# Performance work log

Measured on AMD Instinct MI355X. Metric: run time of the kernel, lower is better.

## Reference

```python
import jax, jax.numpy as jnp
import numpy as np

N_NODES = 8192
N_FEATURES = 512
EMB = 128
N_HEADS = 4
EPS = 1e-6


def setup_inputs() -> dict:
    key = jax.random.key(0)
    k1, k2, k3 = jax.random.split(key, 3)
    X = jax.random.normal(k1, (N_NODES, N_FEATURES), dtype=jnp.float32)
    W = jax.random.normal(k2, (N_FEATURES, EMB), dtype=jnp.float32)
    Z = jax.random.normal(k3, (N_HEADS, N_NODES, EMB), dtype=jnp.float32)
    beta = jnp.ones((), dtype=jnp.float32)
    return {"X": X, "W": W, "Z": Z, "beta": beta}


def reference(X, W, Z, beta):
    # DenseLayer: node embedding
    X_emb = X @ W                                   # [N, E]
    # AffinityLayer: Z @ X_emb^T then cosine-style normalization
    aff = jnp.einsum('hne,me->hnm', Z, X_emb)       # [H, N, N]
    X_norm = jnp.linalg.norm(X_emb, axis=-1)        # [N]
    Z_norm = jnp.linalg.norm(Z, axis=-1)            # [H, N]
    aff = aff / (X_norm[None, None, :] + EPS)
    aff = aff / (Z_norm[:, :, None] + EPS)
    # PoolingLayer: max over heads
    aff = jnp.max(aff, axis=0)                      # [N, N]
    # undirected -> symmetrize
    aff = (aff + aff.T) / 2.0
    # ScalingLayer: map [-1,1] -> [0,1]
    aff = (aff + 1.0) / 2.0
    # ExponentiationLayer
    aff = jnp.power(aff, beta)
    return aff
```

## Files before the change

kernel.cpp:

```cpp
#include <hip/hip_runtime.h>
#include <stdint.h>
#include <stddef.h>

#define N_NODES 8192
#define N_FEAT  512
#define EMB     128
#define N_HEADS 4
#define TILE    128
#define TG      (N_NODES / TILE)
#define NPAIR   (TG * (TG + 1) / 2)
#define TILE_ELEMS (TILE * EMB)

typedef __attribute__((ext_vector_type(8)))  short bf16x8;
typedef __attribute__((ext_vector_type(16))) float f32x16;

__device__ __forceinline__ unsigned short f2bf(float f) {
  union { float f; unsigned int u; } x; x.f = f;
  unsigned int r = (x.u + 0x7FFFu + ((x.u >> 16) & 1u)) >> 16;
  return (unsigned short)r;
}
__device__ __forceinline__ float bf2f(unsigned short u) {
  union { unsigned int u; float f; } x; x.u = ((unsigned int)u) << 16;
  return x.f;
}

__device__ __forceinline__ void gl_lds16(const unsigned short* g, unsigned short* l) {
  __builtin_amdgcn_global_load_lds(
      (__attribute__((address_space(1))) void*)(void*)g,
      (__attribute__((address_space(3))) void*)l, 16, 0, 0);
}

__device__ __forceinline__ int swz_off(int r, int c) {
  int kc = c >> 3;
  return r * EMB + (((kc ^ (r & 7)) << 3) | (c & 7));
}

__device__ __forceinline__ int tidx(int r, int c) {
  int m = (r & 31) ^ ((r & 4) << 2);
  return r * 128 + (c ^ m);
}

__global__ void __launch_bounds__(512) xw_kernel(const float* __restrict__ X,
                                                 const float* __restrict__ W,
                                                 unsigned short* __restrict__ Xen) {
  __shared__ float xs[32][N_FEAT];
  const int t = threadIdx.x;
  const int row0 = blockIdx.x * 32;
#pragma unroll
  for (int i = 0; i < 8; ++i) {
    int e4 = i * 512 + t;
    int row = e4 >> 7;
    int col = (e4 & 127) * 4;
    *(float4*)&xs[row][col] = *(const float4*)&X[(size_t)(row0 + row) * N_FEAT + col];
  }
  __syncthreads();
  const int c0 = (t & 31) * 4;
  const int r0 = (t >> 5) * 2;
  float a00=0.f,a01=0.f,a02=0.f,a03=0.f,a10=0.f,a11=0.f,a12=0.f,a13=0.f;
  for (int k = 0; k < N_FEAT; k += 2) {
    float4 w0 = *(const float4*)&W[(size_t)k * EMB + c0];
    float4 w1 = *(const float4*)&W[(size_t)(k + 1) * EMB + c0];
    float x00 = xs[r0][k],     x01 = xs[r0][k + 1];
    float x10 = xs[r0 + 1][k], x11 = xs[r0 + 1][k + 1];
    a00 += x00*w0.x; a01 += x00*w0.y; a02 += x00*w0.z; a03 += x00*w0.w;
    a10 += x10*w0.x; a11 += x10*w0.y; a12 += x10*w0.z; a13 += x10*w0.w;
    a00 += x01*w1.x; a01 += x01*w1.y; a02 += x01*w1.z; a03 += x01*w1.w;
    a10 += x11*w1.x; a11 += x11*w1.y; a12 += x11*w1.z; a13 += x11*w1.w;
  }
  float s0 = a00*a00 + a01*a01 + a02*a02 + a03*a03;
  float s1 = a10*a10 + a11*a11 + a12*a12 + a13*a13;
#pragma unroll
  for (int off = 16; off >= 1; off >>= 1) {
    s0 += __shfl_xor(s0, off);
    s1 += __shfl_xor(s1, off);
  }
  float inv0 = 1.0f / (sqrtf(s0) + 1e-6f);
  float inv1 = 1.0f / (sqrtf(s1) + 1e-6f);
  union { unsigned short u[4]; uint2 v; } o0, o1;
  o0.u[0]=f2bf(a00*inv0); o0.u[1]=f2bf(a01*inv0); o0.u[2]=f2bf(a02*inv0); o0.u[3]=f2bf(a03*inv0);
  o1.u[0]=f2bf(a10*inv1); o1.u[1]=f2bf(a11*inv1); o1.u[2]=f2bf(a12*inv1); o1.u[3]=f2bf(a13*inv1);
  int n0 = row0 + r0;
  int t0 = n0 >> 7, rr0 = n0 & 127;
  int t1 = (n0 + 1) >> 7, rr1 = (n0 + 1) & 127;
  *(uint2*)&Xen[(size_t)t0 * TILE_ELEMS + swz_off(rr0, c0)] = o0.v;
  *(uint2*)&Xen[(size_t)t1 * TILE_ELEMS + swz_off(rr1, c0)] = o1.v;
}

__global__ void __launch_bounds__(256) znorm_kernel(const float* __restrict__ in,
                                                    unsigned short* __restrict__ out) {
  const int row = blockIdx.x * 4 + (threadIdx.x >> 6);
  const int lane = threadIdx.x & 63;
  float2 v = *(const float2*)&in[(size_t)row * EMB + lane * 2];
  float ss = v.x * v.x + v.y * v.y;
#pragma unroll
  for (int off = 32; off >= 1; off >>= 1) ss += __shfl_xor(ss, off);
  const float s = 1.0f / (sqrtf(ss) + 1e-6f);
  union { unsigned short u[2]; unsigned int w; } o;
  o.u[0] = f2bf(v.x * s);
  o.u[1] = f2bf(v.y * s);
  int tile = row >> 7, r = row & 127, c = lane * 2;
  *(unsigned int*)&out[(size_t)tile * TILE_ELEMS + swz_off(r, c)] = o.w;
}

__device__ __forceinline__ void stageZ(unsigned short* dstLds, const unsigned short* src,
                                       int wid, int lane) {
#pragma unroll
  for (int i = 0; i < 4; ++i) {
    int cbase = i * 512 + wid * 64;
    gl_lds16(src + (size_t)(cbase + lane) * 8, dstLds + (size_t)cbase * 8);
  }
}

__device__ __forceinline__ void do_stage(const unsigned short* cur, const bf16x8 (&XB)[8],
                                         f32x16 (&M)[2], int R0, int fr, int fh) {
  f32x16 acc0 = {}, acc1 = {};
  const int rb = R0 + fr;
  const int sw = rb & 7;
  const unsigned short* base0 = cur + rb * EMB;
#pragma unroll
  for (int kk = 0; kk < 8; ++kk) {
    int kc = kk * 2 + fh;
    int off = ((kc ^ sw) << 3);
    bf16x8 a0 = *(const bf16x8*)(base0 + off);
    bf16x8 a1 = *(const bf16x8*)(base0 + 32 * EMB + off);
    acc0 = __builtin_amdgcn_mfma_f32_32x32x16_bf16(a0, XB[kk], acc0, 0, 0, 0);
    acc1 = __builtin_amdgcn_mfma_f32_32x32x16_bf16(a1, XB[kk], acc1, 0, 0, 0);
  }
#pragma unroll
  for (int q = 0; q < 16; ++q) {
    M[0][q] = fmaxf(M[0][q], acc0[q]);
    M[1][q] = fmaxf(M[1][q], acc1[q]);
  }
}

__global__ void __launch_bounds__(512, 1) affinity_kernel(const unsigned short* __restrict__ Xen,
                                                          const unsigned short* __restrict__ Zn,
                                                          const float* __restrict__ betap,
                                                          float* __restrict__ out) {
  __shared__ __align__(16) unsigned short Zb[2][TILE_ELEMS];
  unsigned short* Tb = &Zb[0][0];

  int bid = blockIdx.x;
  int p = (bid & 7) * (NPAIR / 8) + (bid >> 3);
  int i = (int)(((float)(2 * TG + 1) -
                 sqrtf((float)((2 * TG + 1) * (2 * TG + 1) - 8 * p))) * 0.5f);
  if (i < 0) i = 0;
  if (i > TG - 1) i = TG - 1;
  while (i > 0 && i * TG - i * (i - 1) / 2 > p) --i;
  while ((i + 1) * TG - (i + 1) * i / 2 <= p) ++i;
  const int bi = i;
  const int bj = i + (p - (i * TG - i * (i - 1) / 2));
  const bool diag = (bi == bj);
  const int NS = diag ? 4 : 8;

  const int t = threadIdx.x;
  const int lane = t & 63;
  const int wid = t >> 6;
  const int R0 = (wid >> 2) * 64;
  const int C0 = (wid & 3) * 32;
  const int fr = lane & 31;
  const int fh = lane >> 5;

  stageZ(Zb[0], Zn + ((size_t)(0 * TG + bi) << 14), wid, lane);

  bf16x8 XjB[8], XiB[8];
  {
    const unsigned short* xj = Xen + ((size_t)bj << 14);
    const int r = C0 + fr;
    const int sw = r & 7;
#pragma unroll
    for (int kk = 0; kk < 8; ++kk) {
      int kc = kk * 2 + fh;
      XjB[kk] = *(const bf16x8*)&xj[r * EMB + ((kc ^ sw) << 3)];
    }
    if (!diag) {
      const unsigned short* xi = Xen + ((size_t)bi << 14);
#pragma unroll
      for (int kk = 0; kk < 8; ++kk) {
        int kc = kk * 2 + fh;
        XiB[kk] = *(const bf16x8*)&xi[r * EMB + ((kc ^ sw) << 3)];
      }
    }
  }

  f32x16 maxI[2], maxJ[2];
#pragma unroll
  for (int q = 0; q < 16; ++q) {
    maxI[0][q] = -3.0e38f; maxI[1][q] = -3.0e38f;
    maxJ[0][q] = -3.0e38f; maxJ[1][q] = -3.0e38f;
  }

  __syncthreads();

#pragma unroll
  for (int s = 0; s < 4; ++s) {
    if (s + 1 < NS) {
      int h = (s + 1) & 3;
      int tl = (s + 1 < 4) ? bi : bj;
      stageZ(Zb[(s + 1) & 1], Zn + ((size_t)(h * TG + tl) << 14), wid, lane);
    }
    do_stage(Zb[s & 1], XjB, maxI, R0, fr, fh);
    __syncthreads();
  }
  if (!diag) {
#pragma unroll
    for (int s = 4; s < 8; ++s) {
      if (s < 7) {
        int h = (s + 1) & 3;
        stageZ(Zb[(s + 1) & 1], Zn + ((size_t)(h * TG + bj) << 14), wid, lane);
      }
      do_stage(Zb[s & 1], XiB, maxJ, R0, fr, fh);
      __syncthreads();
    }
  }

#pragma unroll
  for (int ma = 0; ma < 2; ++ma)
#pragma unroll
    for (int q = 0; q < 16; ++q) {
      int r = R0 + ma * 32 + (q & 3) + 8 * (q >> 2) + 4 * fh;
      int c = C0 + fr;
      Tb[tidx(r, c)] = f2bf(diag ? maxI[ma][q] : maxJ[ma][q]);
    }
  __syncthreads();

  const float beta = betap[0];
  const bool bp = (beta != 1.0f);
  float vv[2][16];
#pragma unroll
  for (int ma = 0; ma < 2; ++ma)
#pragma unroll
    for (int q = 0; q < 16; ++q) {
      int r = R0 + ma * 32 + (q & 3) + 8 * (q >> 2) + 4 * fh;
      int c = C0 + fr;
      float a = maxI[ma][q];
      float b = bf2f(Tb[tidx(c, r)]);
      float v = 0.25f * (a + b) + 0.5f;
      if (bp) v = powf(v, beta);
      out[(size_t)(bi * TILE + r) * N_NODES + (size_t)(bj * TILE + c)] = v;
      vv[ma][q] = v;
    }

  if (!diag) {
    __syncthreads();
#pragma unroll
    for (int ma = 0; ma < 2; ++ma)
#pragma unroll
      for (int q = 0; q < 16; ++q) {
        int r = R0 + ma * 32 + (q & 3) + 8 * (q >> 2) + 4 * fh;
        int c = C0 + fr;
        Tb[tidx(c, r)] = f2bf(vv[ma][q]);
      }
    __syncthreads();
#pragma unroll
    for (int it = 0; it < 32; ++it) {
      int row = it * 4 + (t >> 7);
      int col = t & 127;
      out[(size_t)(bj * TILE + row) * N_NODES + (size_t)(bi * TILE + col)] =
          bf2f(Tb[tidx(row, col)]);
    }
  }
}

extern "C" void kernel_launch(void* const* d_in, const int* in_sizes, int n_in,
                              void* d_out, int out_size, void* d_ws, size_t ws_size,
                              hipStream_t stream) {
  const float* X = (const float*)d_in[0];
  const float* W = (const float*)d_in[1];
  const float* Z = (const float*)d_in[2];
  const float* beta = (const float*)d_in[3];
  float* out = (float*)d_out;
  char* ws = (char*)d_ws;

  unsigned short* Xen = (unsigned short*)ws;
  unsigned short* Zn  = (unsigned short*)(ws + (2u << 20));

  hipLaunchKernelGGL(xw_kernel, dim3(N_NODES / 32), dim3(512), 0, stream, X, W, Xen);
  hipLaunchKernelGGL(znorm_kernel, dim3(N_HEADS * N_NODES / 4), dim3(256), 0, stream, Z, Zn);
  hipLaunchKernelGGL(affinity_kernel, dim3(NPAIR), dim3(512), 0, stream, Xen, Zn, beta, out);
}
```

Before: 183.0 us.

## Load Z fragments directly into registers, drop LDS staging, raise occupancy

```diff
diff --git a/kernel.cpp b/kernel.cpp
--- a/kernel.cpp
+++ b/kernel.cpp
@@ -9,7 +9,6 @@
 #define TILE    128
 #define TG      (N_NODES / TILE)
 #define NPAIR   (TG * (TG + 1) / 2)
-#define TILE_ELEMS (TILE * EMB)
 
 typedef __attribute__((ext_vector_type(8)))  short bf16x8;
 typedef __attribute__((ext_vector_type(16))) float f32x16;
@@ -22,17 +21,6 @@
 __device__ __forceinline__ float bf2f(unsigned short u) {
   union { unsigned int u; float f; } x; x.u = ((unsigned int)u) << 16;
   return x.f;
-}
-
-__device__ __forceinline__ void gl_lds16(const unsigned short* g, unsigned short* l) {
-  __builtin_amdgcn_global_load_lds(
-      (__attribute__((address_space(1))) void*)(void*)g,
-      (__attribute__((address_space(3))) void*)l, 16, 0, 0);
-}
-
-__device__ __forceinline__ int swz_off(int r, int c) {
-  int kc = c >> 3;
-  return r * EMB + (((kc ^ (r & 7)) << 3) | (c & 7));
 }
 
 __device__ __forceinline__ int tidx(int r, int c) {
@@ -80,10 +68,8 @@
   o0.u[0]=f2bf(a00*inv0); o0.u[1]=f2bf(a01*inv0); o0.u[2]=f2bf(a02*inv0); o0.u[3]=f2bf(a03*inv0);
   o1.u[0]=f2bf(a10*inv1); o1.u[1]=f2bf(a11*inv1); o1.u[2]=f2bf(a12*inv1); o1.u[3]=f2bf(a13*inv1);
   int n0 = row0 + r0;
-  int t0 = n0 >> 7, rr0 = n0 & 127;
-  int t1 = (n0 + 1) >> 7, rr1 = (n0 + 1) & 127;
-  *(uint2*)&Xen[(size_t)t0 * TILE_ELEMS + swz_off(rr0, c0)] = o0.v;
-  *(uint2*)&Xen[(size_t)t1 * TILE_ELEMS + swz_off(rr1, c0)] = o1.v;
+  *(uint2*)&Xen[(size_t)n0 * EMB + c0] = o0.v;
+  *(uint2*)&Xen[(size_t)(n0 + 1) * EMB + c0] = o1.v;
 }
 
 __global__ void __launch_bounds__(256) znorm_kernel(const float* __restrict__ in,
@@ -98,47 +84,15 @@
   union { unsigned short u[2]; unsigned int w; } o;
   o.u[0] = f2bf(v.x * s);
   o.u[1] = f2bf(v.y * s);
-  int tile = row >> 7, r = row & 127, c = lane * 2;
-  *(unsigned int*)&out[(size_t)tile * TILE_ELEMS + swz_off(r, c)] = o.w;
-}
-
-__device__ __forceinline__ void stageZ(unsigned short* dstLds, const unsigned short* src,
-                                       int wid, int lane) {
-#pragma unroll
-  for (int i = 0; i < 4; ++i) {
-    int cbase = i * 512 + wid * 64;
-    gl_lds16(src + (size_t)(cbase + lane) * 8, dstLds + (size_t)cbase * 8);
-  }
-}
-
-__device__ __forceinline__ void do_stage(const unsigned short* cur, const bf16x8 (&XB)[8],
-                                         f32x16 (&M)[2], int R0, int fr, int fh) {
-  f32x16 acc0 = {}, acc1 = {};
-  const int rb = R0 + fr;
-  const int sw = rb & 7;
-  const unsigned short* base0 = cur + rb * EMB;
-#pragma unroll
-  for (int kk = 0; kk < 8; ++kk) {
-    int kc = kk * 2 + fh;
-    int off = ((kc ^ sw) << 3);
-    bf16x8 a0 = *(const bf16x8*)(base0 + off);
-    bf16x8 a1 = *(const bf16x8*)(base0 + 32 * EMB + off);
-    acc0 = __builtin_amdgcn_mfma_f32_32x32x16_bf16(a0, XB[kk], acc0, 0, 0, 0);
-    acc1 = __builtin_amdgcn_mfma_f32_32x32x16_bf16(a1, XB[kk], acc1, 0, 0, 0);
-  }
-#pragma unroll
-  for (int q = 0; q < 16; ++q) {
-    M[0][q] = fmaxf(M[0][q], acc0[q]);
-    M[1][q] = fmaxf(M[1][q], acc1[q]);
-  }
-}
-
-__global__ void __launch_bounds__(512, 1) affinity_kernel(const unsigned short* __restrict__ Xen,
-                                                          const unsigned short* __restrict__ Zn,
-                                                          const float* __restrict__ betap,
-                                                          float* __restrict__ out) {
-  __shared__ __align__(16) unsigned short Zb[2][TILE_ELEMS];
-  unsigned short* Tb = &Zb[0][0];
+  *(unsigned int*)&out[(size_t)row * EMB + lane * 2] = o.w;
+}
+
+__global__ void __launch_bounds__(512, 2)
+affinity_kernel(const unsigned short* __restrict__ Xen,
+                const unsigned short* __restrict__ Zn,
+                const float* __restrict__ betap,
+                float* __restrict__ out) {
+  __shared__ unsigned short Tb[TILE * TILE];
 
   int bid = blockIdx.x;
   int p = (bid & 7) * (NPAIR / 8) + (bid >> 3);
@@ -151,76 +105,112 @@
   const int bi = i;
   const int bj = i + (p - (i * TG - i * (i - 1) / 2));
   const bool diag = (bi == bj);
-  const int NS = diag ? 4 : 8;
 
   const int t = threadIdx.x;
   const int lane = t & 63;
   const int wid = t >> 6;
-  const int R0 = (wid >> 2) * 64;
-  const int C0 = (wid & 3) * 32;
+  const int R0 = (wid >> 1) * 32;
+  const int C0 = (wid & 1) * 64;
   const int fr = lane & 31;
   const int fh = lane >> 5;
-
-  stageZ(Zb[0], Zn + ((size_t)(0 * TG + bi) << 14), wid, lane);
-
-  bf16x8 XjB[8], XiB[8];
+  const int koff = fh * 8;
+
+  const size_t HSTRIDE = (size_t)N_NODES * EMB;
+  const size_t zi_base = (size_t)bi * TILE * EMB;
+  const size_t zj_base = (size_t)bj * TILE * EMB;
+  const int arow  = (R0 + fr) * EMB + koff;
+  const int xrow0 = (C0 + fr) * EMB + koff;
+  const int xrow1 = (C0 + 32 + fr) * EMB + koff;
+
+  bf16x8 XB0[8], XB1[8];
   {
-    const unsigned short* xj = Xen + ((size_t)bj << 14);
-    const int r = C0 + fr;
-    const int sw = r & 7;
+    const unsigned short* xj = Xen + zj_base;
 #pragma unroll
     for (int kk = 0; kk < 8; ++kk) {
-      int kc = kk * 2 + fh;
-      XjB[kk] = *(const bf16x8*)&xj[r * EMB + ((kc ^ sw) << 3)];
-    }
-    if (!diag) {
-      const unsigned short* xi = Xen + ((size_t)bi << 14);
+      XB0[kk] = *(const bf16x8*)&xj[xrow0 + kk * 16];
+      XB1[kk] = *(const bf16x8*)&xj[xrow1 + kk * 16];
+    }
+  }
+
+  bf16x8 A0[8], A1[8];
+#pragma unroll
+  for (int kk = 0; kk < 8; ++kk)
+    A0[kk] = *(const bf16x8*)&Zn[zi_base + arow + kk * 16];
+
+  f32x16 maxI0, maxI1;
+#pragma unroll
+  for (int q = 0; q < 16; ++q) { maxI0[q] = -3.0e38f; maxI1[q] = -3.0e38f; }
+
+#pragma unroll
+  for (int s = 0; s < 4; ++s) {
+    bf16x8 (&cur)[8] = (s & 1) ? A1 : A0;
+    bf16x8 (&nxt)[8] = (s & 1) ? A0 : A1;
+    if (s < 3) {
+      const unsigned short* nsrc = Zn + (size_t)(s + 1) * HSTRIDE + zi_base;
+#pragma unroll
+      for (int kk = 0; kk < 8; ++kk) nxt[kk] = *(const bf16x8*)&nsrc[arow + kk * 16];
+    } else if (!diag) {
+      const unsigned short* nsrc = Zn + zj_base;
+#pragma unroll
+      for (int kk = 0; kk < 8; ++kk) nxt[kk] = *(const bf16x8*)&nsrc[arow + kk * 16];
+    }
+    f32x16 acc0 = {}, acc1 = {};
+#pragma unroll
+    for (int kk = 0; kk < 8; ++kk) {
+      acc0 = __builtin_amdgcn_mfma_f32_32x32x16_bf16(cur[kk], XB0[kk], acc0, 0, 0, 0);
+      acc1 = __builtin_amdgcn_mfma_f32_32x32x16_bf16(cur[kk], XB1[kk], acc1, 0, 0, 0);
+    }
+#pragma unroll
+    for (int q = 0; q < 16; ++q) {
+      maxI0[q] = fmaxf(maxI0[q], acc0[q]);
+      maxI1[q] = fmaxf(maxI1[q], acc1[q]);
+    }
+  }
+
+  f32x16 maxJ0, maxJ1;
+#pragma unroll
+  for (int q = 0; q < 16; ++q) { maxJ0[q] = -3.0e38f; maxJ1[q] = -3.0e38f; }
+
+  if (!diag) {
+    const unsigned short* xi = Xen + zi_base;
+#pragma unroll
+    for (int kk = 0; kk < 8; ++kk) {
+      XB0[kk] = *(const bf16x8*)&xi[xrow0 + kk * 16];
+      XB1[kk] = *(const bf16x8*)&xi[xrow1 + kk * 16];
+    }
+#pragma unroll
+    for (int s = 0; s < 4; ++s) {
+      bf16x8 (&cur)[8] = (s & 1) ? A1 : A0;
+      bf16x8 (&nxt)[8] = (s & 1) ? A0 : A1;
+      if (s < 3) {
+        const unsigned short* nsrc = Zn + (size_t)(s + 1) * HSTRIDE + zj_base;
+#pragma unroll
+        for (int kk = 0; kk < 8; ++kk) nxt[kk] = *(const bf16x8*)&nsrc[arow + kk * 16];
+      }
+      f32x16 acc0 = {}, acc1 = {};
 #pragma unroll
       for (int kk = 0; kk < 8; ++kk) {
-        int kc = kk * 2 + fh;
-        XiB[kk] = *(const bf16x8*)&xi[r * EMB + ((kc ^ sw) << 3)];
-      }
-    }
-  }
-
-  f32x16 maxI[2], maxJ[2];
-#pragma unroll
-  for (int q = 0; q < 16; ++q) {
-    maxI[0][q] = -3.0e38f; maxI[1][q] = -3.0e38f;
-    maxJ[0][q] = -3.0e38f; maxJ[1][q] = -3.0e38f;
-  }
-
-  __syncthreads();
-
-#pragma unroll
-  for (int s = 0; s < 4; ++s) {
-    if (s + 1 < NS) {
-      int h = (s + 1) & 3;
-      int tl = (s + 1 < 4) ? bi : bj;
-      stageZ(Zb[(s + 1) & 1], Zn + ((size_t)(h * TG + tl) << 14), wid, lane);
-    }
-    do_stage(Zb[s & 1], XjB, maxI, R0, fr, fh);
-    __syncthreads();
-  }
-  if (!diag) {
-#pragma unroll
-    for (int s = 4; s < 8; ++s) {
-      if (s < 7) {
-        int h = (s + 1) & 3;
-        stageZ(Zb[(s + 1) & 1], Zn + ((size_t)(h * TG + bj) << 14), wid, lane);
-      }
-      do_stage(Zb[s & 1], XiB, maxJ, R0, fr, fh);
-      __syncthreads();
-    }
-  }
-
-#pragma unroll
-  for (int ma = 0; ma < 2; ++ma)
+        acc0 = __builtin_amdgcn_mfma_f32_32x32x16_bf16(cur[kk], XB0[kk], acc0, 0, 0, 0);
+        acc1 = __builtin_amdgcn_mfma_f32_32x32x16_bf16(cur[kk], XB1[kk], acc1, 0, 0, 0);
+      }
+#pragma unroll
+      for (int q = 0; q < 16; ++q) {
+        maxJ0[q] = fmaxf(maxJ0[q], acc0[q]);
+        maxJ1[q] = fmaxf(maxJ1[q], acc1[q]);
+      }
+    }
+  }
+
+#pragma unroll
+  for (int nb = 0; nb < 2; ++nb)
 #pragma unroll
     for (int q = 0; q < 16; ++q) {
-      int r = R0 + ma * 32 + (q & 3) + 8 * (q >> 2) + 4 * fh;
-      int c = C0 + fr;
-      Tb[tidx(r, c)] = f2bf(diag ? maxI[ma][q] : maxJ[ma][q]);
+      int r = R0 + (q & 3) + 8 * (q >> 2) + 4 * fh;
+      int c = C0 + nb * 32 + fr;
+      float v;
+      if (diag)      v = nb ? maxI1[q] : maxI0[q];
+      else           v = nb ? maxJ1[q] : maxJ0[q];
+      Tb[tidx(r, c)] = f2bf(v);
     }
   __syncthreads();
 
@@ -228,36 +218,38 @@
   const bool bp = (beta != 1.0f);
   float vv[2][16];
 #pragma unroll
-  for (int ma = 0; ma < 2; ++ma)
+  for (int nb = 0; nb < 2; ++nb)
 #pragma unroll
     for (int q = 0; q < 16; ++q) {
-      int r = R0 + ma * 32 + (q & 3) + 8 * (q >> 2) + 4 * fh;
-      int c = C0 + fr;
-      float a = maxI[ma][q];
+      int r = R0 + (q & 3) + 8 * (q >> 2) + 4 * fh;
+      int c = C0 + nb * 32 + fr;
+      float a = nb ? maxI1[q] : maxI0[q];
       float b = bf2f(Tb[tidx(c, r)]);
       float v = 0.25f * (a + b) + 0.5f;
       if (bp) v = powf(v, beta);
-      out[(size_t)(bi * TILE + r) * N_NODES + (size_t)(bj * TILE + c)] = v;
-      vv[ma][q] = v;
+      __builtin_nontemporal_store(
+          v, &out[(size_t)(bi * TILE + r) * N_NODES + (size_t)(bj * TILE + c)]);
+      vv[nb][q] = v;
     }
 
   if (!diag) {
     __syncthreads();
 #pragma unroll
-    for (int ma = 0; ma < 2; ++ma)
+    for (int nb = 0; nb < 2; ++nb)
 #pragma unroll
       for (int q = 0; q < 16; ++q) {
-        int r = R0 + ma * 32 + (q & 3) + 8 * (q >> 2) + 4 * fh;
-        int c = C0 + fr;
-        Tb[tidx(c, r)] = f2bf(vv[ma][q]);
+        int r = R0 + (q & 3) + 8 * (q >> 2) + 4 * fh;
+        int c = C0 + nb * 32 + fr;
+        Tb[tidx(c, r)] = f2bf(vv[nb][q]);
       }
     __syncthreads();
 #pragma unroll
     for (int it = 0; it < 32; ++it) {
       int row = it * 4 + (t >> 7);
       int col = t & 127;
-      out[(size_t)(bj * TILE + row) * N_NODES + (size_t)(bi * TILE + col)] =
-          bf2f(Tb[tidx(row, col)]);
+      __builtin_nontemporal_store(
+          bf2f(Tb[tidx(row, col)]),
+          &out[(size_t)(bj * TILE + row) * N_NODES + (size_t)(bi * TILE + col)]);
     }
   }
 }
```

Result: slower. 484.3 us (+164.7%).
